# Optimization experiments

Hardware: AMD Instinct MI355X
Metric: run time of the kernel (lower is better)

The kernel has to match this reference:

```python
import jax, jax.numpy as jnp
import numpy as np

B, N, E, A, H, F, HEADS = 2, 16384, 262144, 3, 128, 16, 4
DH = H // HEADS
CONST = (2.0 * np.pi) ** 0.5


def setup_inputs() -> dict:
    key = jax.random.key(0)
    ks = jax.random.split(key, 16)
    s = 0.05
    return {
        "x": jax.random.normal(ks[0], (B, N, H), jnp.float32),
        "edge_index": jax.random.randint(ks[1], (2, E), 0, N),
        # per-action message MLPs (self.mlp)
        "mlp_W1": jax.random.normal(ks[2], (A, H, H), jnp.float32) * s,
        "mlp_b1": jnp.zeros((A, H), jnp.float32),
        "mlp_W2": jax.random.normal(ks[3], (A, H, H), jnp.float32) * s,
        "mlp_b2": jnp.zeros((A, H), jnp.float32),
        # transformer (MMTs) projections, 4 heads over the action axis
        "Wq": jax.random.normal(ks[4], (H, H), jnp.float32) * s,
        "bq": jnp.zeros((H,), jnp.float32),
        "Wk": jax.random.normal(ks[5], (H, H), jnp.float32) * s,
        "bk": jnp.zeros((H,), jnp.float32),
        "Wv": jax.random.normal(ks[6], (H, H), jnp.float32) * s,
        "bv": jnp.zeros((H,), jnp.float32),
        "Wo": jax.random.normal(ks[7], (H, H), jnp.float32) * s,
        "bo": jnp.zeros((H,), jnp.float32),
        # decide_mu MLPs (decide_In_sigma is never used in the original forward)
        "mu_W1": jax.random.normal(ks[8], (A, H, H), jnp.float32) * s,
        "mu_b1": jnp.zeros((A, H), jnp.float32),
        "mu_W2": jax.random.normal(ks[9], (A, H, F), jnp.float32) * s,
        "mu_b2": jnp.zeros((A, F), jnp.float32),
    }


def _forward(x, edge_index, mlp_W1, mlp_b1, mlp_W2, mlp_b2,
             Wq, bq, Wk, bk, Wv, bv, Wo, bo, mu_W1, mu_b1, mu_W2, mu_b2):
    # per-action MLP stack: (B,N,H) -> (B,N,A,H)
    h = jax.nn.relu(jnp.einsum('bnh,ahk->bnak', x, mlp_W1) + mlp_b1)
    h = jnp.einsum('bnak,akh->bnah', h, mlp_W2) + mlp_b2
    # gather along source nodes, scatter-add into destination bins
    dst, src = edge_index[0], edge_index[1]
    g = h[:, src]                                   # (B,E,A,H) ~ 800 MB
    agg = jax.ops.segment_sum(jnp.moveaxis(g, 1, 0), dst, num_segments=N)
    agg = jnp.moveaxis(agg, 0, 1)                   # (B,N,A,H)
    # multi-head self-attention over the action axis (len A) per node
    q = (jnp.einsum('bnah,hk->bnak', agg, Wq) + bq).reshape(B, N, A, HEADS, DH)
    k = (jnp.einsum('bnah,hk->bnak', agg, Wk) + bk).reshape(B, N, A, HEADS, DH)
    v = (jnp.einsum('bnah,hk->bnak', agg, Wv) + bv).reshape(B, N, A, HEADS, DH)
    scores = jnp.einsum('bnqed,bnked->bneqk', q, k) / (DH ** 0.5)
    attn = jax.nn.softmax(scores, axis=-1)
    o = jnp.einsum('bneqk,bnked->bnqed', attn, v).reshape(B, N, A, H)
    h_I = agg + jnp.einsum('bnah,hk->bnak', o, Wo) + bo  # residual
    # per-action decode to action means: (B,N,A,F)
    m = jax.nn.relu(jnp.einsum('bnah,ahk->bnak', h_I, mu_W1) + mu_b1)
    mu = jnp.einsum('bnak,akf->bnaf', m, mu_W2) + mu_b2
    # Gaussian reparameterized sampling, VAR is a non-trainable all-ones buffer
    VAR = jnp.ones((N, A, F), jnp.float32)
    noise = jax.random.normal(jax.random.key(42), mu.shape, mu.dtype)
    sample = mu + noise * VAR
    logp = -jnp.log(CONST * VAR) - (sample - mu) ** 2 / (2.0 * VAR ** 2)
    a0 = jax.nn.softmax(jnp.tanh(sample[:, :, 0, :]), axis=-1)
    a1 = jax.nn.sigmoid(sample[:, :, 1, :])
    a2 = jnp.tanh(sample[:, :, 2, :])
    sample_out = jnp.stack([a0, a1, a2], axis=2)    # (B,N,A,F)
    return sample_out, logp.sum((-1, -2))           # ((B,N,A,F),(B,N))


def reference(x, edge_index, mlp_W1, mlp_b1, mlp_W2, mlp_b2,
              Wq, bq, Wk, bk, Wv, bv, Wo, bo, mu_W1, mu_b1, mu_W2, mu_b2):
    return _forward(x, edge_index, mlp_W1, mlp_b1, mlp_W2, mlp_b2,
                    Wq, bq, Wk, bk, Wv, bv, Wo, bo, mu_W1, mu_b1, mu_W2, mu_b2)
```

## Files before the change

### kernel.cpp

```cpp
#include <hip/hip_runtime.h>
#include <hip/hip_bf16.h>

#define NN    16384
#define EE    262144
#define BNODES 32768
#define AH    384
#define TOT_NOISE 1572864u

typedef __attribute__((ext_vector_type(8))) short short8;
typedef __attribute__((ext_vector_type(4))) float v4f;
typedef __attribute__((ext_vector_type(2))) float f32x2;

__device__ __forceinline__ unsigned short f2bf(float f) {
  unsigned u = __float_as_uint(f);
  unsigned r = u + 0x7fffu + ((u >> 16) & 1u);
  return (unsigned short)(r >> 16);
}
__device__ __forceinline__ float bf2f(unsigned short h) {
  return __uint_as_float(((unsigned)h) << 16);
}
__device__ __forceinline__ float bflo(unsigned u) { return __uint_as_float(u << 16); }
__device__ __forceinline__ float bfhi(unsigned u) { return __uint_as_float(u & 0xffff0000u); }
__device__ __forceinline__ unsigned pk_bf16(float a, float b) {
  __hip_bfloat162 h = __float22bfloat162_rn(make_float2(a, b));
  return *(unsigned*)&h;
}

__device__ __forceinline__ void threefry2x32_042(unsigned& x0, unsigned& x1) {
  const unsigned ks0 = 0u;
  const unsigned ks1 = 42u;
  const unsigned ks2 = 0x1BD11BDAu ^ 0u ^ 42u;
  x0 += ks0; x1 += ks1;
#define TFR(r) { x0 += x1; x1 = (x1 << (r)) | (x1 >> (32 - (r))); x1 ^= x0; }
  TFR(13) TFR(15) TFR(26) TFR(6)   x0 += ks1; x1 += ks2 + 1u;
  TFR(17) TFR(29) TFR(16) TFR(24)  x0 += ks2; x1 += ks0 + 2u;
  TFR(13) TFR(15) TFR(26) TFR(6)   x0 += ks0; x1 += ks1 + 3u;
  TFR(17) TFR(29) TFR(16) TFR(24)  x0 += ks1; x1 += ks2 + 4u;
  TFR(13) TFR(15) TFR(26) TFR(6)   x0 += ks2; x1 += ks0 + 5u;
#undef TFR
}

__device__ __forceinline__ float erfinv_f32(float x) {
  float w = -log1pf(-x * x);
  float p;
  if (w < 5.0f) {
    w -= 2.5f;
    p = 2.81022636e-08f;
    p = fmaf(p, w, 3.43273939e-07f);
    p = fmaf(p, w, -3.5233877e-06f);
    p = fmaf(p, w, -4.39150654e-06f);
    p = fmaf(p, w, 0.00021858087f);
    p = fmaf(p, w, -0.00125372503f);
    p = fmaf(p, w, -0.00417768164f);
    p = fmaf(p, w, 0.246640727f);
    p = fmaf(p, w, 1.50140941f);
  } else {
    w = sqrtf(w) - 3.0f;
    p = -0.000200214257f;
    p = fmaf(p, w, 0.000100950558f);
    p = fmaf(p, w, 0.00134934322f);
    p = fmaf(p, w, -0.00367342844f);
    p = fmaf(p, w, 0.00573950773f);
    p = fmaf(p, w, -0.0076224613f);
    p = fmaf(p, w, 0.00943887047f);
    p = fmaf(p, w, 1.00167406f);
    p = fmaf(p, w, 2.83297682f);
  }
  return p * x;
}

__device__ __forceinline__ unsigned jax_random_bits32(unsigned i) {
  unsigned x0 = 0u, x1 = i;
  threefry2x32_042(x0, x1);
  return x0 ^ x1;
}

__device__ __forceinline__ float jax_normal_from_bits(unsigned bits) {
  float f = __uint_as_float((bits >> 9) | 0x3f800000u) - 1.0f;
  const float lo = -0.99999994f;
  float u = f * 2.0f + lo;
  u = fmaxf(u, lo);
  return 1.4142135623730951f * erfinv_f32(u);
}

__global__ void edge_count(const int* __restrict__ dst, int* __restrict__ deg) {
  int e = blockIdx.x * 256 + threadIdx.x;
  if (e < EE) atomicAdd(&deg[dst[e]], 1);
}

__global__ __launch_bounds__(1024) void scan_k(const int* __restrict__ deg,
                                               int* __restrict__ offs,
                                               int* __restrict__ cur) {
  __shared__ int wsum[16];
  const int t = threadIdx.x;
  const int base = t * 16;
  int loc[16];
  int s = 0;
#pragma unroll
  for (int i = 0; i < 16; i++) { loc[i] = deg[base + i]; s += loc[i]; }
  const int mysum = s;
  const int lane = t & 63, wid = t >> 6;
#pragma unroll
  for (int off = 1; off < 64; off <<= 1) {
    int v = __shfl_up(s, off, 64);
    if (lane >= off) s += v;
  }
  if (lane == 63) wsum[wid] = s;
  __syncthreads();
  if (t == 0) {
    int r = 0;
#pragma unroll
    for (int i = 0; i < 16; i++) { int v = wsum[i]; wsum[i] = r; r += v; }
  }
  __syncthreads();
  int run = wsum[wid] + s - mysum;
#pragma unroll
  for (int i = 0; i < 16; i++) {
    offs[base + i] = run;
    cur[base + i] = run;
    run += loc[i];
  }
  if (t == 1023) offs[NN] = run;
}

__global__ void edge_fill(const int* __restrict__ dst, const int* __restrict__ srcv,
                          int* __restrict__ cur, int* __restrict__ csr) {
  int e = blockIdx.x * 256 + threadIdx.x;
  if (e < EE) {
    int d = dst[e];
    int p = atomicAdd(&cur[d], 1);
    csr[p] = srcv[e];
  }
}

__global__ __launch_bounds__(256) void prep_wfrag(
    const float* __restrict__ W1, const float* __restrict__ W2,
    const float* __restrict__ mW1,
    const float* __restrict__ Wq, const float* __restrict__ Wk,
    const float* __restrict__ Wv, const float* __restrict__ Wo,
    const float* __restrict__ mW2,
    unsigned short* __restrict__ F) {
  int m = blockIdx.y;
  int f = blockIdx.x * 256 + threadIdx.x;
  if (m == 13) {
    if (f < 6144) {
      int a = f >> 11;
      int r2 = f & 2047;
      int kt = r2 >> 9;
      int r = r2 & 511;
      int lane = r >> 3, j = r & 7;
      int k = kt * 32 + (lane >> 4) * 8 + j;
      int n = lane & 15;
      F[13 * 16384 + f] = f2bf(mW2[(a * 128 + k) * 16 + n]);
    }
    return;
  }
  const float* W;
  if (m < 3) W = W1 + (long)m * 16384;
  else if (m < 6) W = W2 + (long)(m - 3) * 16384;
  else if (m < 9) W = mW1 + (long)(m - 6) * 16384;
  else W = (m == 9) ? Wq : (m == 10) ? Wk : (m == 11) ? Wv : Wo;
  int tile = f >> 9;
  int kt = tile >> 3, nt = tile & 7;
  int r = f & 511;
  int lane = r >> 3, j = r & 7;
  int k = kt * 32 + (lane >> 4) * 8 + j;
  int n = nt * 16 + (lane & 15);
  F[(long)m * 16384 + f] = f2bf(W[k * 128 + n]);
}

#define GXSTR 136
__global__ __launch_bounds__(256, 4) void mlp_fused(
    const float* __restrict__ X,
    const unsigned short* __restrict__ WF1, const float* __restrict__ b1,
    const unsigned short* __restrict__ WF2, const float* __restrict__ b2,
    unsigned short* __restrict__ H) {
  __shared__ __align__(16) unsigned short As[128 * GXSTR];
  const int a = blockIdx.y;
  const long m0 = (long)blockIdx.x * 128;
  const int tid = threadIdx.x;
  const unsigned short* Wp1 = WF1 + (long)a * 16384;
  const unsigned short* Wp2 = WF2 + (long)a * 16384;

#pragma unroll
  for (int p = 0; p < 8; p++) {
    int c = tid + p * 256;
    int row = c >> 4, c8 = (c & 15) * 8;
    float4 v1 = *(const float4*)(X + (m0 + row) * 128 + c8);
    float4 v2 = *(const float4*)(X + (m0 + row) * 128 + c8 + 4);
    uint4 o = make_uint4(pk_bf16(v1.x, v1.y), pk_bf16(v1.z, v1.w),
                         pk_bf16(v2.x, v2.y), pk_bf16(v2.z, v2.w));
    *(uint4*)(&As[row * GXSTR + c8]) = o;
  }
  __syncthreads();

  const int w = tid >> 6, l = tid & 63, lr = l & 15, lg = l >> 4;

  v4f acc[8][2];
#pragma unroll
  for (int mt = 0; mt < 8; mt++) {
    acc[mt][0] = (v4f){0.f, 0.f, 0.f, 0.f};
    acc[mt][1] = (v4f){0.f, 0.f, 0.f, 0.f};
  }
#pragma unroll
  for (int kt = 0; kt < 4; kt++) {
    short8 bfr[2];
#pragma unroll
    for (int ntl = 0; ntl < 2; ntl++)
      bfr[ntl] = *(const short8*)(Wp1 + (long)(kt * 8 + 2 * w + ntl) * 512 + l * 8);
#pragma unroll
    for (int mt = 0; mt < 8; mt++) {
      short8 af = *(const short8*)(&As[(mt * 16 + lr) * GXSTR + kt * 32 + lg * 8]);
      acc[mt][0] = __builtin_amdgcn_mfma_f32_16x16x32_bf16(af, bfr[0], acc[mt][0], 0, 0, 0);
      acc[mt][1] = __builtin_amdgcn_mfma_f32_16x16x32_bf16(af, bfr[1], acc[mt][1], 0, 0, 0);
    }
  }
  __syncthreads();

  {
    float bv[2] = {b1[a * 128 + 32 * w + lr], b1[a * 128 + 32 * w + 16 + lr]};
#pragma unroll
    for (int mt = 0; mt < 8; mt++)
#pragma unroll
      for (int ntl = 0; ntl < 2; ntl++)
#pragma unroll
        for (int i = 0; i < 4; i++) {
          int row = mt * 16 + lg * 4 + i;
          int col = 32 * w + ntl * 16 + lr;
          As[row * GXSTR + col] = f2bf(fmaxf(acc[mt][ntl][i] + bv[ntl], 0.0f));
        }
  }
  __syncthreads();

#pragma unroll
  for (int mt = 0; mt < 8; mt++) {
    acc[mt][0] = (v4f){0.f, 0.f, 0.f, 0.f};
    acc[mt][1] = (v4f){0.f, 0.f, 0.f, 0.f};
  }
#pragma unroll
  for (int kt = 0; kt < 4; kt++) {
    short8 bfr[2];
#pragma unroll
    for (int ntl = 0; ntl < 2; ntl++)
      bfr[ntl] = *(const short8*)(Wp2 + (long)(kt * 8 + 2 * w + ntl) * 512 + l * 8);
#pragma unroll
    for (int mt = 0; mt < 8; mt++) {
      short8 af = *(const short8*)(&As[(mt * 16 + lr) * GXSTR + kt * 32 + lg * 8]);
      acc[mt][0] = __builtin_amdgcn_mfma_f32_16x16x32_bf16(af, bfr[0], acc[mt][0], 0, 0, 0);
      acc[mt][1] = __builtin_amdgcn_mfma_f32_16x16x32_bf16(af, bfr[1], acc[mt][1], 0, 0, 0);
    }
  }
  {
    float bv[2] = {b2[a * 128 + 32 * w + lr], b2[a * 128 + 32 * w + 16 + lr]};
#pragma unroll
    for (int mt = 0; mt < 8; mt++)
#pragma unroll
      for (int ntl = 0; ntl < 2; ntl++)
#pragma unroll
        for (int i = 0; i < 4; i++) {
          long row = m0 + mt * 16 + lg * 4 + i;
          int col = 32 * w + ntl * 16 + lr;
          H[row * 384 + a * 128 + col] = f2bf(acc[mt][ntl][i] + bv[ntl]);
        }
  }
}

#define XSTR 136
#define QSTR 34
__global__ __launch_bounds__(256, 3) void attn_mega(
    const unsigned short* __restrict__ H, const int* __restrict__ offs,
    const int* __restrict__ csr,
    const unsigned short* __restrict__ WF,
    const float* __restrict__ bq, const float* __restrict__ bk,
    const float* __restrict__ bv, const float* __restrict__ bo,
    const unsigned short* __restrict__ WM1, const float* __restrict__ mb1,
    const unsigned short* __restrict__ WM2, const float* __restrict__ mb2,
    float* __restrict__ out0, float* __restrict__ out1) {
  __shared__ __align__(16) unsigned short xS[48 * XSTR];
  __shared__ __align__(16) unsigned short kS[4 * 48 * QSTR];
  __shared__ __align__(16) unsigned short vS[4 * 48 * QSTR];
  __shared__ float lpS[48];

  const int tid = threadIdx.x;
  const long node0 = (long)blockIdx.x * 16;

  {
    const int bt = (int)(node0 >> 14);
    const int nbase = (int)(node0 & (NN - 1));
    const int nd = tid >> 4;
    const int sub = tid & 15;
    const int n = nbase + nd;
    const int e0 = offs[n], e1 = offs[n + 1];
    const int cnt = e1 - e0;
    const unsigned short* hb = H + (long)bt * NN * 384 + sub * 24;
    f32x2 acc12[12];
#pragma unroll
    for (int i = 0; i < 12; i++) acc12[i] = (f32x2){0.f, 0.f};

    int i0, i1, i2, i3;
    { int a_ = e0 + sub;      a_ = (a_ < EE) ? a_ : (EE - 1); i0 = csr[a_]; }
    { int a_ = e0 + 16 + sub; a_ = (a_ < EE) ? a_ : (EE - 1); i1 = csr[a_]; }
    { int a_ = e0 + 32 + sub; a_ = (a_ < EE) ? a_ : (EE - 1); i2 = csr[a_]; }
    { int a_ = e0 + 48 + sub; a_ = (a_ < EE) ? a_ : (EE - 1); i3 = csr[a_]; }

#define ACC8(bp, u)                                                     \
    { acc12[bp+0] += (f32x2){bflo(u.x), bfhi(u.x)};                     \
      acc12[bp+1] += (f32x2){bflo(u.y), bfhi(u.y)};                     \
      acc12[bp+2] += (f32x2){bflo(u.z), bfhi(u.z)};                     \
      acc12[bp+3] += (f32x2){bflo(u.w), bfhi(u.w)}; }
#define GACC(BUF, KK)                                                   \
    if ((KK) < cnt) { ACC8(0, BUF##0) ACC8(4, BUF##1) ACC8(8, BUF##2) }
#define ROWLD(BUF, SPTR)                                                \
    { const unsigned short* p_ = hb + (long)(SPTR) * 384;               \
      BUF##0 = *(const uint4*)(p_);                                     \
      BUF##1 = *(const uint4*)(p_ + 8);                                 \
      BUF##2 = *(const uint4*)(p_ + 16); }
#define SWZ(reg, k) __builtin_amdgcn_ds_swizzle(reg, ((k) << 5) | 16)
#define IDXG(reg, k, e) (((e) < cnt) ? SWZ(reg, k) : 0)
#define BLOCK16(b, ic, in)                                              \
    GACC(A, (b)+0)  ROWLD(A, IDXG(ic, 4,  (b)+4))                       \
    GACC(B, (b)+1)  ROWLD(B, IDXG(ic, 5,  (b)+5))                       \
    GACC(C, (b)+2)  ROWLD(C, IDXG(ic, 6,  (b)+6))                       \
    GACC(D, (b)+3)  ROWLD(D, IDXG(ic, 7,  (b)+7))                       \
    GACC(A, (b)+4)  ROWLD(A, IDXG(ic, 8,  (b)+8))                       \
    GACC(B, (b)+5)  ROWLD(B, IDXG(ic, 9,  (b)+9))                       \
    GACC(C, (b)+6)  ROWLD(C, IDXG(ic, 10, (b)+10))                      \
    GACC(D, (b)+7)  ROWLD(D, IDXG(ic, 11, (b)+11))                      \
    GACC(A, (b)+8)  ROWLD(A, IDXG(ic, 12, (b)+12))                      \
    GACC(B, (b)+9)  ROWLD(B, IDXG(ic, 13, (b)+13))                      \
    GACC(C, (b)+10) ROWLD(C, IDXG(ic, 14, (b)+14))                      \
    GACC(D, (b)+11) ROWLD(D, IDXG(ic, 15, (b)+15))                      \
    GACC(A, (b)+12) ROWLD(A, IDXG(in, 0,  (b)+16))                      \
    GACC(B, (b)+13) ROWLD(B, IDXG(in, 1,  (b)+17))                      \
    GACC(C, (b)+14) ROWLD(C, IDXG(in, 2,  (b)+18))                      \
    GACC(D, (b)+15) ROWLD(D, IDXG(in, 3,  (b)+19))

    uint4 A0, A1, A2, B0, B1, B2, C0, C1, C2, D0, D1, D2;
    {
      int t0 = IDXG(i0, 0, 0), t1 = IDXG(i0, 1, 1);
      int t2 = IDXG(i0, 2, 2), t3 = IDXG(i0, 3, 3);
      ROWLD(A, t0) ROWLD(B, t1) ROWLD(C, t2) ROWLD(D, t3)
    }
    BLOCK16(0, i0, i1)
    if (cnt > 16) {
      BLOCK16(16, i1, i2)
      if (cnt > 32) {
        BLOCK16(32, i2, i3)
        if (cnt > 48) {
          BLOCK16(48, i3, i3)
        }
      }
    }
    if (cnt > 64) {
      for (int e = 64; e < cnt; e++) {
        int s0 = csr[e0 + e];
        const unsigned short* p0 = hb + (long)s0 * 384;
        uint4 F0 = *(const uint4*)(p0);
        uint4 F1 = *(const uint4*)(p0 + 8);
        uint4 F2 = *(const uint4*)(p0 + 16);
        ACC8(0, F0) ACC8(4, F1) ACC8(8, F2)
      }
    }
#undef BLOCK16
#undef IDXG
#undef SWZ
#undef ROWLD
#undef GACC
#undef ACC8
#pragma unroll
    for (int jj = 0; jj < 12; jj++) {
      int g = sub * 24 + 2 * jj;
      int a_ = g >> 7;
      int c = g & 127;
      *(unsigned*)&xS[(3 * nd + a_) * XSTR + c] =
          pk_bf16(acc12[jj].x, acc12[jj].y);
    }
  }
  __syncthreads();

  const int w = tid >> 6;
  const int l = tid & 63;
  const int lr = l & 15;
  const int lg = l >> 4;
  const unsigned short* WQ = WF;
  const unsigned short* WK = WF + 16384;
  const unsigned short* WV = WF + 32768;
  const unsigned short* WO = WF + 49152;

  v4f accq[3][2], acck[3][2], accv[3][2];
#pragma unroll
  for (int mt = 0; mt < 3; mt++)
#pragma unroll
    for (int n = 0; n < 2; n++) {
      accq[mt][n] = (v4f){0.f, 0.f, 0.f, 0.f};
      acck[mt][n] = (v4f){0.f, 0.f, 0.f, 0.f};
      accv[mt][n] = (v4f){0.f, 0.f, 0.f, 0.f};
    }
#pragma unroll
  for (int kt = 0; kt < 4; kt++) {
    short8 af[3];
#pragma unroll
    for (int mt = 0; mt < 3; mt++)
      af[mt] = *(const short8*)&xS[(mt * 16 + lr) * XSTR + kt * 32 + lg * 8];
#pragma unroll
    for (int ntl = 0; ntl < 2; ntl++) {
      long tf = (long)(kt * 8 + 2 * w + ntl) * 512 + l * 8;
      short8 b0 = *(const short8*)&WQ[tf];
      short8 b1 = *(const short8*)&WK[tf];
      short8 b2 = *(const short8*)&WV[tf];
#pragma unroll
      for (int mt = 0; mt < 3; mt++) {
        accq[mt][ntl] = __builtin_amdgcn_mfma_f32_16x16x32_bf16(af[mt], b0, accq[mt][ntl], 0, 0, 0);
        acck[mt][ntl] = __builtin_amdgcn_mfma_f32_16x16x32_bf16(af[mt], b1, acck[mt][ntl], 0, 0, 0);
        accv[mt][ntl] = __builtin_amdgcn_mfma_f32_16x16x32_bf16(af[mt], b2, accv[mt][ntl], 0, 0, 0);
      }
    }
  }
  __syncthreads();

  float resv[3][2][4];
#pragma unroll
  for (int mt = 0; mt < 3; mt++)
#pragma unroll
    for (int ntl = 0; ntl < 2; ntl++)
#pragma unroll
      for (int i = 0; i < 4; i++)
        resv[mt][ntl][i] =
            bf2f(xS[(mt * 16 + lg * 4 + i) * XSTR + 32 * w + ntl * 16 + lr]);

  {
    const float scale = 0.17677669529663687f;
    unsigned short* kw = &kS[w * 48 * QSTR];
    unsigned short* vw = &vS[w * 48 * QSTR];
    float bqv[2] = {bq[32 * w + lr], bq[32 * w + 16 + lr]};
    float bkv[2] = {bk[32 * w + lr], bk[32 * w + 16 + lr]};
    float bvv[2] = {bv[32 * w + lr], bv[32 * w + 16 + lr]};
#pragma unroll
    for (int mt = 0; mt < 3; mt++)
#pragma unroll
      for (int ntl = 0; ntl < 2; ntl++)
#pragma unroll
        for (int i = 0; i < 4; i++) {
          int row = mt * 16 + lg * 4 + i;
          int col = ntl * 16 + lr;
          xS[row * XSTR + 32 * w + col] = f2bf((accq[mt][ntl][i] + bqv[ntl]) * scale);
          kw[row * QSTR + col] = f2bf(acck[mt][ntl][i] + bkv[ntl]);
          vw[row * QSTR + col] = f2bf(accv[mt][ntl][i] + bvv[ntl]);
        }
  }
  __syncthreads();

  if (l < 48) {
    int aq = l % 3;
    int ndr = l - aq;
    const unsigned* qr = (const unsigned*)&xS[l * XSTR + 32 * w];
    const unsigned* kr0 = (const unsigned*)&kS[(w * 48 + ndr) * QSTR];
    const unsigned* kr1 = (const unsigned*)&kS[(w * 48 + ndr + 1) * QSTR];
    const unsigned* kr2 = (const unsigned*)&kS[(w * 48 + ndr + 2) * QSTR];
// ... 73 lines not shown
  for (int mt = 0; mt < 3; mt++)
#pragma unroll
    for (int n = 0; n < 2; n++) accm[mt][n] = (v4f){0.f, 0.f, 0.f, 0.f};
#pragma unroll
  for (int kt = 0; kt < 4; kt++) {
#pragma unroll
    for (int mt = 0; mt < 3; mt++) {
      short8 af = *(const short8*)&xS[(mt * 16 + lr) * XSTR + kt * 32 + lg * 8];
#pragma unroll
      for (int ntl = 0; ntl < 2; ntl++) {
        short8 b = *(const short8*)(WM1 + (long)mt * 16384 +
                                    (long)(kt * 8 + 2 * w + ntl) * 512 + l * 8);
        accm[mt][ntl] = __builtin_amdgcn_mfma_f32_16x16x32_bf16(af, b, accm[mt][ntl], 0, 0, 0);
      }
    }
  }
  __syncthreads();

#pragma unroll
  for (int mt = 0; mt < 3; mt++)
#pragma unroll
    for (int ntl = 0; ntl < 2; ntl++) {
      int col = 32 * w + ntl * 16 + lr;
      float bias = mb1[mt * 128 + col];
#pragma unroll
      for (int i = 0; i < 4; i++) {
        int rowp = mt * 16 + lg * 4 + i;
        xS[rowp * XSTR + col] = f2bf(fmaxf(accm[mt][ntl][i] + bias, 0.0f));
      }
    }
  __syncthreads();

  if (w < 3) {
    v4f accu = (v4f){0.f, 0.f, 0.f, 0.f};
#pragma unroll
    for (int kt = 0; kt < 4; kt++) {
      short8 af = *(const short8*)&xS[(w * 16 + lr) * XSTR + kt * 32 + lg * 8];
      short8 b = *(const short8*)(WM2 + w * 2048 + kt * 512 + l * 8);
      accu = __builtin_amdgcn_mfma_f32_16x16x32_bf16(af, b, accu, 0, 0, 0);
    }
    float bias = mb2[w * 16 + lr];
#pragma unroll
    for (int i = 0; i < 4; i++) {
      int nd = lg * 4 + i;
      float mu = accu[i] + bias;
      unsigned gidx = (unsigned)((node0 + nd) * 48 + w * 16 + lr);
      unsigned bits = jax_random_bits32(gidx);
      float noise = jax_normal_from_bits(bits);
      float sample = mu + noise;
      float lp = -0.9189385332046727f - 0.5f * noise * noise;
      lp += __shfl_xor(lp, 1, 64);
      lp += __shfl_xor(lp, 2, 64);
      lp += __shfl_xor(lp, 4, 64);
      lp += __shfl_xor(lp, 8, 64);
      if (lr == 0) lpS[w * 16 + nd] = lp;
      float res;
      if (w == 0) {
        float th = tanhf(sample);
        float mx = th;
        mx = fmaxf(mx, __shfl_xor(mx, 1, 64));
        mx = fmaxf(mx, __shfl_xor(mx, 2, 64));
        mx = fmaxf(mx, __shfl_xor(mx, 4, 64));
        mx = fmaxf(mx, __shfl_xor(mx, 8, 64));
        float ex = expf(th - mx);
        float ss = ex;
        ss += __shfl_xor(ss, 1, 64);
        ss += __shfl_xor(ss, 2, 64);
        ss += __shfl_xor(ss, 4, 64);
        ss += __shfl_xor(ss, 8, 64);
        res = ex / ss;
      } else if (w == 1) {
        res = 1.0f / (1.0f + expf(-sample));
      } else {
        res = tanhf(sample);
      }
      out0[gidx] = res;
    }
  }
  __syncthreads();
  if (tid < 16)
    out1[node0 + tid] = lpS[tid] + lpS[16 + tid] + lpS[32 + tid];
}

extern "C" void kernel_launch(void* const* d_in, const int* in_sizes, int n_in,
                              void* d_out, int out_size, void* d_ws, size_t ws_size,
                              hipStream_t stream) {
  const float* x = (const float*)d_in[0];
  const int* ei = (const int*)d_in[1];
  const float* W1 = (const float*)d_in[2];
  const float* b1 = (const float*)d_in[3];
  const float* W2 = (const float*)d_in[4];
  const float* b2 = (const float*)d_in[5];
  const float* Wq = (const float*)d_in[6];
  const float* bq = (const float*)d_in[7];
  const float* Wk = (const float*)d_in[8];
  const float* bk = (const float*)d_in[9];
  const float* Wv = (const float*)d_in[10];
  const float* bv = (const float*)d_in[11];
  const float* Wo = (const float*)d_in[12];
  const float* bo = (const float*)d_in[13];
  const float* mW1 = (const float*)d_in[14];
  const float* mb1 = (const float*)d_in[15];
  const float* mW2 = (const float*)d_in[16];
  const float* mb2 = (const float*)d_in[17];
  (void)in_sizes; (void)n_in; (void)out_size; (void)ws_size;

  unsigned short* HB = (unsigned short*)d_ws;
  int* deg = (int*)(HB + 12582912);
  int* offs = deg + NN;
  int* cur = offs + (NN + 1);
  int* csr = cur + NN;
  unsigned short* wfrag = (unsigned short*)(((uintptr_t)(csr + EE) + 15) & ~(uintptr_t)15);
  unsigned short* w2frag = wfrag + 13 * 16384;

  const int* dst = ei;
  const int* srcv = ei + EE;

  float* out0 = (float*)d_out;
  float* out1 = out0 + TOT_NOISE;

  hipMemsetAsync(deg, 0, NN * sizeof(int), stream);
  edge_count<<<EE / 256, 256, 0, stream>>>(dst, deg);
  scan_k<<<1, 1024, 0, stream>>>(deg, offs, cur);
  edge_fill<<<EE / 256, 256, 0, stream>>>(dst, srcv, cur, csr);
  prep_wfrag<<<dim3(64, 14), 256, 0, stream>>>(W1, W2, mW1, Wq, Wk, Wv, Wo, mW2, wfrag);

  mlp_fused<<<dim3(BNODES / 128, 3), 256, 0, stream>>>(x, wfrag, b1, wfrag + 3 * 16384, b2, HB);
  attn_mega<<<BNODES / 16, 256, 0, stream>>>(HB, offs, csr,
                                             wfrag + 9 * 16384, bq, bk, bv, bo,
                                             wfrag + 6 * 16384, mb1, w2frag, mb2,
                                             out0, out1);
}
```

Measured before the change: 225.8 us.

## Split gather from attention kernel to raise gather occupancy

Splits the fused gather+attention kernel into a standalone gather kernel, launch-bounded for 8 blocks per CU with a shallower 2-deep load pipeline, and a post kernel that reads the aggregated bf16 rows from a new workspace buffer. The aim is to let the latency-bound random gather run at higher occupancy instead of being capped by the attention kernel's register and LDS use. In exchange, the aggregate (about 25 MB in bf16) makes an extra round trip through global memory and there is one more launch. The fused kernel is kept as a fallback when the workspace is too small.

```diff
diff --git a/kernel.cpp b/kernel.cpp
--- a/kernel.cpp
+++ b/kernel.cpp
@@ -265,43 +265,26 @@
   }
 }
 
-#define XSTR 136
-#define QSTR 34
-__global__ __launch_bounds__(256, 3) void attn_mega(
+__global__ __launch_bounds__(256, 8) void gather_k(
     const unsigned short* __restrict__ H, const int* __restrict__ offs,
-    const int* __restrict__ csr,
-    const unsigned short* __restrict__ WF,
-    const float* __restrict__ bq, const float* __restrict__ bk,
-    const float* __restrict__ bv, const float* __restrict__ bo,
-    const unsigned short* __restrict__ WM1, const float* __restrict__ mb1,
-    const unsigned short* __restrict__ WM2, const float* __restrict__ mb2,
-    float* __restrict__ out0, float* __restrict__ out1) {
-  __shared__ __align__(16) unsigned short xS[48 * XSTR];
-  __shared__ __align__(16) unsigned short kS[4 * 48 * QSTR];
-  __shared__ __align__(16) unsigned short vS[4 * 48 * QSTR];
-  __shared__ float lpS[48];
-
+    const int* __restrict__ csr, unsigned short* __restrict__ AGG) {
   const int tid = threadIdx.x;
   const long node0 = (long)blockIdx.x * 16;
-
-  {
-    const int bt = (int)(node0 >> 14);
-    const int nbase = (int)(node0 & (NN - 1));
-    const int nd = tid >> 4;
-    const int sub = tid & 15;
-    const int n = nbase + nd;
-    const int e0 = offs[n], e1 = offs[n + 1];
-    const int cnt = e1 - e0;
-    const unsigned short* hb = H + (long)bt * NN * 384 + sub * 24;
-    f32x2 acc12[12];
-#pragma unroll
-    for (int i = 0; i < 12; i++) acc12[i] = (f32x2){0.f, 0.f};
-
-    int i0, i1, i2, i3;
-    { int a_ = e0 + sub;      a_ = (a_ < EE) ? a_ : (EE - 1); i0 = csr[a_]; }
-    { int a_ = e0 + 16 + sub; a_ = (a_ < EE) ? a_ : (EE - 1); i1 = csr[a_]; }
-    { int a_ = e0 + 32 + sub; a_ = (a_ < EE) ? a_ : (EE - 1); i2 = csr[a_]; }
-    { int a_ = e0 + 48 + sub; a_ = (a_ < EE) ? a_ : (EE - 1); i3 = csr[a_]; }
+  const int bt = (int)(node0 >> 14);
+  const int nbase = (int)(node0 & (NN - 1));
+  const int nd = tid >> 4;
+  const int sub = tid & 15;
+  const int n = nbase + nd;
+  const int e0 = offs[n], e1 = offs[n + 1];
+  const int cnt = e1 - e0;
+  const unsigned short* hb = H + (long)bt * NN * 384 + sub * 24;
+  f32x2 acc12[12];
+#pragma unroll
+  for (int i = 0; i < 12; i++) acc12[i] = (f32x2){0.f, 0.f};
+
+  int i0, i1;
+  { int a_ = e0 + sub;      a_ = (a_ < EE) ? a_ : (EE - 1); i0 = csr[a_]; }
+  { int a_ = e0 + 16 + sub; a_ = (a_ < EE) ? a_ : (EE - 1); i1 = csr[a_]; }
 
 #define ACC8(bp, u)                                                     \
     { acc12[bp+0] += (f32x2){bflo(u.x), bfhi(u.x)};                     \
@@ -317,42 +300,34 @@
       BUF##2 = *(const uint4*)(p_ + 16); }
 #define SWZ(reg, k) __builtin_amdgcn_ds_swizzle(reg, ((k) << 5) | 16)
 #define IDXG(reg, k, e) (((e) < cnt) ? SWZ(reg, k) : 0)
-#define BLOCK16(b, ic, in)                                              \
-    GACC(A, (b)+0)  ROWLD(A, IDXG(ic, 4,  (b)+4))                       \
-    GACC(B, (b)+1)  ROWLD(B, IDXG(ic, 5,  (b)+5))                       \
-    GACC(C, (b)+2)  ROWLD(C, IDXG(ic, 6,  (b)+6))                       \
-    GACC(D, (b)+3)  ROWLD(D, IDXG(ic, 7,  (b)+7))                       \
-    GACC(A, (b)+4)  ROWLD(A, IDXG(ic, 8,  (b)+8))                       \
-    GACC(B, (b)+5)  ROWLD(B, IDXG(ic, 9,  (b)+9))                       \
-    GACC(C, (b)+6)  ROWLD(C, IDXG(ic, 10, (b)+10))                      \
-    GACC(D, (b)+7)  ROWLD(D, IDXG(ic, 11, (b)+11))                      \
-    GACC(A, (b)+8)  ROWLD(A, IDXG(ic, 12, (b)+12))                      \
-    GACC(B, (b)+9)  ROWLD(B, IDXG(ic, 13, (b)+13))                      \
-    GACC(C, (b)+10) ROWLD(C, IDXG(ic, 14, (b)+14))                      \
-    GACC(D, (b)+11) ROWLD(D, IDXG(ic, 15, (b)+15))                      \
-    GACC(A, (b)+12) ROWLD(A, IDXG(in, 0,  (b)+16))                      \
-    GACC(B, (b)+13) ROWLD(B, IDXG(in, 1,  (b)+17))                      \
-    GACC(C, (b)+14) ROWLD(C, IDXG(in, 2,  (b)+18))                      \
-    GACC(D, (b)+15) ROWLD(D, IDXG(in, 3,  (b)+19))
-
-    uint4 A0, A1, A2, B0, B1, B2, C0, C1, C2, D0, D1, D2;
-    {
-      int t0 = IDXG(i0, 0, 0), t1 = IDXG(i0, 1, 1);
-      int t2 = IDXG(i0, 2, 2), t3 = IDXG(i0, 3, 3);
-      ROWLD(A, t0) ROWLD(B, t1) ROWLD(C, t2) ROWLD(D, t3)
-    }
-    BLOCK16(0, i0, i1)
-    if (cnt > 16) {
-      BLOCK16(16, i1, i2)
-      if (cnt > 32) {
-        BLOCK16(32, i2, i3)
-        if (cnt > 48) {
-          BLOCK16(48, i3, i3)
-        }
-      }
-    }
-    if (cnt > 64) {
-      for (int e = 64; e < cnt; e++) {
+#define BLOCK16_D2(b, ic, in)                                           \
+    GACC(A, (b)+0)  ROWLD(A, IDXG(ic, 2,  (b)+2))                       \
+    GACC(B, (b)+1)  ROWLD(B, IDXG(ic, 3,  (b)+3))                       \
+    GACC(A, (b)+2)  ROWLD(A, IDXG(ic, 4,  (b)+4))                       \
+    GACC(B, (b)+3)  ROWLD(B, IDXG(ic, 5,  (b)+5))                       \
+    GACC(A, (b)+4)  ROWLD(A, IDXG(ic, 6,  (b)+6))                       \
+    GACC(B, (b)+5)  ROWLD(B, IDXG(ic, 7,  (b)+7))                       \
+    GACC(A, (b)+6)  ROWLD(A, IDXG(ic, 8,  (b)+8))                       \
+    GACC(B, (b)+7)  ROWLD(B, IDXG(ic, 9,  (b)+9))                       \
+    GACC(A, (b)+8)  ROWLD(A, IDXG(ic, 10, (b)+10))                      \
+    GACC(B, (b)+9)  ROWLD(B, IDXG(ic, 11, (b)+11))                      \
+    GACC(A, (b)+10) ROWLD(A, IDXG(ic, 12, (b)+12))                      \
+    GACC(B, (b)+11) ROWLD(B, IDXG(ic, 13, (b)+13))                      \
+    GACC(A, (b)+12) ROWLD(A, IDXG(ic, 14, (b)+14))                      \
+    GACC(B, (b)+13) ROWLD(B, IDXG(ic, 15, (b)+15))                      \
+    GACC(A, (b)+14) ROWLD(A, IDXG(in, 0,  (b)+16))                      \
+    GACC(B, (b)+15) ROWLD(B, IDXG(in, 1,  (b)+17))
+
+  uint4 A0, A1, A2, B0, B1, B2;
+  {
+    int t0 = IDXG(i0, 0, 0), t1 = IDXG(i0, 1, 1);
+    ROWLD(A, t0) ROWLD(B, t1)
+  }
+  BLOCK16_D2(0, i0, i1)
+  if (cnt > 16) {
+    BLOCK16_D2(16, i1, i1)
+    if (cnt > 32) {
+      for (int e = 32; e < cnt; e++) {
         int s0 = csr[e0 + e];
         const unsigned short* p0 = hb + (long)s0 * 384;
         uint4 F0 = *(const uint4*)(p0);
@@ -361,19 +336,66 @@
         ACC8(0, F0) ACC8(4, F1) ACC8(8, F2)
       }
     }
-#undef BLOCK16
+  }
+#undef BLOCK16_D2
 #undef IDXG
 #undef SWZ
 #undef ROWLD
 #undef GACC
 #undef ACC8
+
+  uint4 o0 = make_uint4(pk_bf16(acc12[0].x, acc12[0].y),
+                        pk_bf16(acc12[1].x, acc12[1].y),
+                        pk_bf16(acc12[2].x, acc12[2].y),
+                        pk_bf16(acc12[3].x, acc12[3].y));
+  uint4 o1 = make_uint4(pk_bf16(acc12[4].x, acc12[4].y),
+                        pk_bf16(acc12[5].x, acc12[5].y),
+                        pk_bf16(acc12[6].x, acc12[6].y),
+                        pk_bf16(acc12[7].x, acc12[7].y));
+  uint4 o2 = make_uint4(pk_bf16(acc12[8].x, acc12[8].y),
+                        pk_bf16(acc12[9].x, acc12[9].y),
+                        pk_bf16(acc12[10].x, acc12[10].y),
+                        pk_bf16(acc12[11].x, acc12[11].y));
+  unsigned short* op = AGG + (node0 + (long)nd) * 384 + sub * 24;
+  *(uint4*)(op) = o0;
+  *(uint4*)(op + 8) = o1;
+  *(uint4*)(op + 16) = o2;
+}
+
+#define XSTR 136
+#define QSTR 34
+__global__ __launch_bounds__(256, 3) void attn_post(
+    const unsigned short* __restrict__ AGG,
+    const unsigned short* __restrict__ WF,
+    const float* __restrict__ bq, const float* __restrict__ bk,
+    const float* __restrict__ bv, const float* __restrict__ bo,
+    const unsigned short* __restrict__ WM1, const float* __restrict__ mb1,
+    const unsigned short* __restrict__ WM2, const float* __restrict__ mb2,
+    float* __restrict__ out0, float* __restrict__ out1) {
+  __shared__ __align__(16) unsigned short xS[48 * XSTR];
+  __shared__ __align__(16) unsigned short kS[4 * 48 * QSTR];
+  __shared__ __align__(16) unsigned short vS[4 * 48 * QSTR];
+  __shared__ float lpS[48];
+
+  const int tid = threadIdx.x;
+  const long node0 = (long)blockIdx.x * 16;
+
+  {
+    const int nd = tid >> 4;
+    const int sub = tid & 15;
+    const unsigned short* ag = AGG + (node0 + (long)nd) * 384 + sub * 24;
+    uint4 r0 = *(const uint4*)(ag);
+    uint4 r1 = *(const uint4*)(ag + 8);
+    uint4 r2 = *(const uint4*)(ag + 16);
+    unsigned pr[12] = {r0.x, r0.y, r0.z, r0.w,
+                       r1.x, r1.y, r1.z, r1.w,
+                       r2.x, r2.y, r2.z, r2.w};
 #pragma unroll
     for (int jj = 0; jj < 12; jj++) {
       int g = sub * 24 + 2 * jj;
       int a_ = g >> 7;
       int c = g & 127;
-      *(unsigned*)&xS[(3 * nd + a_) * XSTR + c] =
-          pk_bf16(acc12[jj].x, acc12[jj].y);
+      *(unsigned*)&xS[(3 * nd + a_) * XSTR + c] = pr[jj];
     }
   }
   __syncthreads();
@@ -613,6 +635,352 @@
     out1[node0 + tid] = lpS[tid] + lpS[16 + tid] + lpS[32 + tid];
 }
 
+__global__ __launch_bounds__(256, 3) void attn_mega(
+    const unsigned short* __restrict__ H, const int* __restrict__ offs,
+    const int* __restrict__ csr,
+    const unsigned short* __restrict__ WF,
+    const float* __restrict__ bq, const float* __restrict__ bk,
+    const float* __restrict__ bv, const float* __restrict__ bo,
+    const unsigned short* __restrict__ WM1, const float* __restrict__ mb1,
+    const unsigned short* __restrict__ WM2, const float* __restrict__ mb2,
+    float* __restrict__ out0, float* __restrict__ out1) {
+  __shared__ __align__(16) unsigned short xS[48 * XSTR];
+  __shared__ __align__(16) unsigned short kS[4 * 48 * QSTR];
+  __shared__ __align__(16) unsigned short vS[4 * 48 * QSTR];
+  __shared__ float lpS[48];
+
+  const int tid = threadIdx.x;
+  const long node0 = (long)blockIdx.x * 16;
+
+  {
+    const int bt = (int)(node0 >> 14);
+    const int nbase = (int)(node0 & (NN - 1));
+    const int nd = tid >> 4;
+    const int sub = tid & 15;
+    const int n = nbase + nd;
+    const int e0 = offs[n], e1 = offs[n + 1];
+    const int cnt = e1 - e0;
+    const unsigned short* hb = H + (long)bt * NN * 384 + sub * 24;
+    f32x2 acc12[12];
+#pragma unroll
+    for (int i = 0; i < 12; i++) acc12[i] = (f32x2){0.f, 0.f};
+
+    int i0, i1, i2, i3;
+    { int a_ = e0 + sub;      a_ = (a_ < EE) ? a_ : (EE - 1); i0 = csr[a_]; }
+    { int a_ = e0 + 16 + sub; a_ = (a_ < EE) ? a_ : (EE - 1); i1 = csr[a_]; }
+    { int a_ = e0 + 32 + sub; a_ = (a_ < EE) ? a_ : (EE - 1); i2 = csr[a_]; }
+    { int a_ = e0 + 48 + sub; a_ = (a_ < EE) ? a_ : (EE - 1); i3 = csr[a_]; }
+
+#define ACC8(bp, u)                                                     \
+    { acc12[bp+0] += (f32x2){bflo(u.x), bfhi(u.x)};                     \
+      acc12[bp+1] += (f32x2){bflo(u.y), bfhi(u.y)};                     \
+      acc12[bp+2] += (f32x2){bflo(u.z), bfhi(u.z)};                     \
+      acc12[bp+3] += (f32x2){bflo(u.w), bfhi(u.w)}; }
+#define GACC(BUF, KK)                                                   \
+    if ((KK) < cnt) { ACC8(0, BUF##0) ACC8(4, BUF##1) ACC8(8, BUF##2) }
+#define ROWLD(BUF, SPTR)                                                \
+    { const unsigned short* p_ = hb + (long)(SPTR) * 384;               \
+      BUF##0 = *(const uint4*)(p_);                                     \
+      BUF##1 = *(const uint4*)(p_ + 8);                                 \
+      BUF##2 = *(const uint4*)(p_ + 16); }
+#define SWZ(reg, k) __builtin_amdgcn_ds_swizzle(reg, ((k) << 5) | 16)
+#define IDXG(reg, k, e) (((e) < cnt) ? SWZ(reg, k) : 0)
+#define BLOCK16(b, ic, in)                                              \
+    GACC(A, (b)+0)  ROWLD(A, IDXG(ic, 4,  (b)+4))                       \
+    GACC(B, (b)+1)  ROWLD(B, IDXG(ic, 5,  (b)+5))                       \
+    GACC(C, (b)+2)  ROWLD(C, IDXG(ic, 6,  (b)+6))                       \
+    GACC(D, (b)+3)  ROWLD(D, IDXG(ic, 7,  (b)+7))                       \
+    GACC(A, (b)+4)  ROWLD(A, IDXG(ic, 8,  (b)+8))                       \
+    GACC(B, (b)+5)  ROWLD(B, IDXG(ic, 9,  (b)+9))                       \
+    GACC(C, (b)+6)  ROWLD(C, IDXG(ic, 10, (b)+10))                      \
+    GACC(D, (b)+7)  ROWLD(D, IDXG(ic, 11, (b)+11))                      \
+    GACC(A, (b)+8)  ROWLD(A, IDXG(ic, 12, (b)+12))                      \
+    GACC(B, (b)+9)  ROWLD(B, IDXG(ic, 13, (b)+13))                      \
+    GACC(C, (b)+10) ROWLD(C, IDXG(ic, 14, (b)+14))                      \
+    GACC(D, (b)+11) ROWLD(D, IDXG(ic, 15, (b)+15))                      \
+    GACC(A, (b)+12) ROWLD(A, IDXG(in, 0,  (b)+16))                      \
+    GACC(B, (b)+13) ROWLD(B, IDXG(in, 1,  (b)+17))                      \
+    GACC(C, (b)+14) ROWLD(C, IDXG(in, 2,  (b)+18))                      \
+    GACC(D, (b)+15) ROWLD(D, IDXG(in, 3,  (b)+19))
+
+    uint4 A0, A1, A2, B0, B1, B2, C0, C1, C2, D0, D1, D2;
+    {
+      int t0 = IDXG(i0, 0, 0), t1 = IDXG(i0, 1, 1);
+      int t2 = IDXG(i0, 2, 2), t3 = IDXG(i0, 3, 3);
+      ROWLD(A, t0) ROWLD(B, t1) ROWLD(C, t2) ROWLD(D, t3)
+    }
+    BLOCK16(0, i0, i1)
+    if (cnt > 16) {
+      BLOCK16(16, i1, i2)
+      if (cnt > 32) {
+        BLOCK16(32, i2, i3)
+        if (cnt > 48) {
+          BLOCK16(48, i3, i3)
+        }
+      }
+    }
+    if (cnt > 64) {
+      for (int e = 64; e < cnt; e++) {
+        int s0 = csr[e0 + e];
+        const unsigned short* p0 = hb + (long)s0 * 384;
+        uint4 F0 = *(const uint4*)(p0);
+        uint4 F1 = *(const uint4*)(p0 + 8);
+        uint4 F2 = *(const uint4*)(p0 + 16);
+        ACC8(0, F0) ACC8(4, F1) ACC8(8, F2)
+      }
+    }
+#undef BLOCK16
+#undef IDXG
+#undef SWZ
+#undef ROWLD
+#undef GACC
+#undef ACC8
+#pragma unroll
+    for (int jj = 0; jj < 12; jj++) {
+      int g = sub * 24 + 2 * jj;
+      int a_ = g >> 7;
+      int c = g & 127;
+      *(unsigned*)&xS[(3 * nd + a_) * XSTR + c] =
+          pk_bf16(acc12[jj].x, acc12[jj].y);
+    }
+  }
+  __syncthreads();
+
+  const int w = tid >> 6;
+  const int l = tid & 63;
+  const int lr = l & 15;
+  const int lg = l >> 4;
+  const unsigned short* WQ = WF;
+  const unsigned short* WK = WF + 16384;
+  const unsigned short* WV = WF + 32768;
+  const unsigned short* WO = WF + 49152;
+
+  v4f accq[3][2], acck[3][2], accv[3][2];
+#pragma unroll
+  for (int mt = 0; mt < 3; mt++)
+#pragma unroll
+    for (int n = 0; n < 2; n++) {
+      accq[mt][n] = (v4f){0.f, 0.f, 0.f, 0.f};
+      acck[mt][n] = (v4f){0.f, 0.f, 0.f, 0.f};
+      accv[mt][n] = (v4f){0.f, 0.f, 0.f, 0.f};
+    }
+#pragma unroll
+  for (int kt = 0; kt < 4; kt++) {
+    short8 af[3];
+#pragma unroll
+    for (int mt = 0; mt < 3; mt++)
+      af[mt] = *(const short8*)&xS[(mt * 16 + lr) * XSTR + kt * 32 + lg * 8];
+#pragma unroll
+    for (int ntl = 0; ntl < 2; ntl++) {
+      long tf = (long)(kt * 8 + 2 * w + ntl) * 512 + l * 8;
+      short8 b0 = *(const short8*)&WQ[tf];
+      short8 b1 = *(const short8*)&WK[tf];
+      short8 b2 = *(const short8*)&WV[tf];
+#pragma unroll
+      for (int mt = 0; mt < 3; mt++) {
+        accq[mt][ntl] = __builtin_amdgcn_mfma_f32_16x16x32_bf16(af[mt], b0, accq[mt][ntl], 0, 0, 0);
+        acck[mt][ntl] = __builtin_amdgcn_mfma_f32_16x16x32_bf16(af[mt], b1, acck[mt][ntl], 0, 0, 0);
+        accv[mt][ntl] = __builtin_amdgcn_mfma_f32_16x16x32_bf16(af[mt], b2, accv[mt][ntl], 0, 0, 0);
+      }
+    }
+  }
+  __syncthreads();
+
+  float resv[3][2][4];
+#pragma unroll
+  for (int mt = 0; mt < 3; mt++)
+#pragma unroll
+    for (int ntl = 0; ntl < 2; ntl++)
+#pragma unroll
+      for (int i = 0; i < 4; i++)
+        resv[mt][ntl][i] =
+            bf2f(xS[(mt * 16 + lg * 4 + i) * XSTR + 32 * w + ntl * 16 + lr]);
+
+  {
+    const float scale = 0.17677669529663687f;
+    unsigned short* kw = &kS[w * 48 * QSTR];
+    unsigned short* vw = &vS[w * 48 * QSTR];
+    float bqv[2] = {bq[32 * w + lr], bq[32 * w + 16 + lr]};
+    float bkv[2] = {bk[32 * w + lr], bk[32 * w + 16 + lr]};
+    float bvv[2] = {bv[32 * w + lr], bv[32 * w + 16 + lr]};
+#pragma unroll
+    for (int mt = 0; mt < 3; mt++)
+#pragma unroll
+      for (int ntl = 0; ntl < 2; ntl++)
+#pragma unroll
+        for (int i = 0; i < 4; i++) {
+          int row = mt * 16 + lg * 4 + i;
+          int col = ntl * 16 + lr;
+          xS[row * XSTR + 32 * w + col] = f2bf((accq[mt][ntl][i] + bqv[ntl]) * scale);
+          kw[row * QSTR + col] = f2bf(acck[mt][ntl][i] + bkv[ntl]);
+          vw[row * QSTR + col] = f2bf(accv[mt][ntl][i] + bvv[ntl]);
+        }
+  }
+  __syncthreads();
+
+  if (l < 48) {
+    int aq = l % 3;
+    int ndr = l - aq;
+    const unsigned* qr = (const unsigned*)&xS[l * XSTR + 32 * w];
+    const unsigned* kr0 = (const unsigned*)&kS[(w * 48 + ndr) * QSTR];
+    const unsigned* kr1 = (const unsigned*)&kS[(w * 48 + ndr + 1) * QSTR];
+    const unsigned* kr2 = (const unsigned*)&kS[(w * 48 + ndr + 2) * QSTR];
+    float s0 = 0.f, s1 = 0.f, s2 = 0.f;
+#pragma unroll
+    for (int j = 0; j < 16; j++) {
+      unsigned uq = qr[j], u0 = kr0[j], u1 = kr1[j], u2 = kr2[j];
+      float qa = bflo(uq), qb = bfhi(uq);
+      s0 = fmaf(qa, bflo(u0), fmaf(qb, bfhi(u0), s0));
+      s1 = fmaf(qa, bflo(u1), fmaf(qb, bfhi(u1), s1));
+      s2 = fmaf(qa, bflo(u2), fmaf(qb, bfhi(u2), s2));
+    }
+    float mx = fmaxf(s0, fmaxf(s1, s2));
+    float e0 = expf(s0 - mx), e1 = expf(s1 - mx), e2 = expf(s2 - mx);
+    float inv = 1.0f / (e0 + e1 + e2);
+    e0 *= inv; e1 *= inv; e2 *= inv;
+    const unsigned* vr0 = (const unsigned*)&vS[(w * 48 + ndr) * QSTR];
+    const unsigned* vr1 = (const unsigned*)&vS[(w * 48 + ndr + 1) * QSTR];
+    const unsigned* vr2 = (const unsigned*)&vS[(w * 48 + ndr + 2) * QSTR];
+    unsigned ov[16];
+#pragma unroll
+    for (int j = 0; j < 16; j++) {
+      unsigned u0 = vr0[j], u1 = vr1[j], u2 = vr2[j];
+      float oa = fmaf(e0, bflo(u0), fmaf(e1, bflo(u1), e2 * bflo(u2)));
+      float ob = fmaf(e0, bfhi(u0), fmaf(e1, bfhi(u1), e2 * bfhi(u2)));
+      ov[j] = pk_bf16(oa, ob);
+    }
+    uint4* orow = (uint4*)&xS[l * XSTR + 32 * w];
+    orow[0] = make_uint4(ov[0], ov[1], ov[2], ov[3]);
+    orow[1] = make_uint4(ov[4], ov[5], ov[6], ov[7]);
+    orow[2] = make_uint4(ov[8], ov[9], ov[10], ov[11]);
+    orow[3] = make_uint4(ov[12], ov[13], ov[14], ov[15]);
+  }
+  __syncthreads();
+
+  v4f acco[3][2];
+#pragma unroll
+  for (int mt = 0; mt < 3; mt++)
+#pragma unroll
+    for (int n = 0; n < 2; n++) acco[mt][n] = (v4f){0.f, 0.f, 0.f, 0.f};
+#pragma unroll
+  for (int kt = 0; kt < 4; kt++) {
+    short8 af[3];
+#pragma unroll
+    for (int mt = 0; mt < 3; mt++)
+      af[mt] = *(const short8*)&xS[(mt * 16 + lr) * XSTR + kt * 32 + lg * 8];
+#pragma unroll
+    for (int ntl = 0; ntl < 2; ntl++) {
+      long tf = (long)(kt * 8 + 2 * w + ntl) * 512 + l * 8;
+      short8 b = *(const short8*)&WO[tf];
+#pragma unroll
+      for (int mt = 0; mt < 3; mt++)
+        acco[mt][ntl] = __builtin_amdgcn_mfma_f32_16x16x32_bf16(af[mt], b, acco[mt][ntl], 0, 0, 0);
+    }
+  }
+  __syncthreads();
+
+  {
+    float bov[2] = {bo[32 * w + lr], bo[32 * w + 16 + lr]};
+#pragma unroll
+    for (int mt = 0; mt < 3; mt++)
+#pragma unroll
+      for (int ntl = 0; ntl < 2; ntl++)
+#pragma unroll
+        for (int i = 0; i < 4; i++) {
+          int row = mt * 16 + lg * 4 + i;
+          int nd = row / 3, a_ = row - nd * 3;
+          int gcol = 32 * w + ntl * 16 + lr;
+          xS[(a_ * 16 + nd) * XSTR + gcol] =
+              f2bf(acco[mt][ntl][i] + bov[ntl] + resv[mt][ntl][i]);
+        }
+  }
+  __syncthreads();
+
+  v4f accm[3][2];
+#pragma unroll
+  for (int mt = 0; mt < 3; mt++)
+#pragma unroll
+    for (int n = 0; n < 2; n++) accm[mt][n] = (v4f){0.f, 0.f, 0.f, 0.f};
+#pragma unroll
+  for (int kt = 0; kt < 4; kt++) {
+#pragma unroll
+    for (int mt = 0; mt < 3; mt++) {
+      short8 af = *(const short8*)&xS[(mt * 16 + lr) * XSTR + kt * 32 + lg * 8];
+#pragma unroll
+      for (int ntl = 0; ntl < 2; ntl++) {
+        short8 b = *(const short8*)(WM1 + (long)mt * 16384 +
+                                    (long)(kt * 8 + 2 * w + ntl) * 512 + l * 8);
+        accm[mt][ntl] = __builtin_amdgcn_mfma_f32_16x16x32_bf16(af, b, accm[mt][ntl], 0, 0, 0);
+      }
+    }
+  }
+  __syncthreads();
+
+#pragma unroll
+  for (int mt = 0; mt < 3; mt++)
+#pragma unroll
+    for (int ntl = 0; ntl < 2; ntl++) {
+      int col = 32 * w + ntl * 16 + lr;
+      float bias = mb1[mt * 128 + col];
+#pragma unroll
+      for (int i = 0; i < 4; i++) {
+        int rowp = mt * 16 + lg * 4 + i;
+        xS[rowp * XSTR + col] = f2bf(fmaxf(accm[mt][ntl][i] + bias, 0.0f));
+      }
+    }
+  __syncthreads();
+
+  if (w < 3) {
+    v4f accu = (v4f){0.f, 0.f, 0.f, 0.f};
+#pragma unroll
+    for (int kt = 0; kt < 4; kt++) {
+      short8 af = *(const short8*)&xS[(w * 16 + lr) * XSTR + kt * 32 + lg * 8];
+      short8 b = *(const short8*)(WM2 + w * 2048 + kt * 512 + l * 8);
+      accu = __builtin_amdgcn_mfma_f32_16x16x32_bf16(af, b, accu, 0, 0, 0);
+    }
+    float bias = mb2[w * 16 + lr];
+#pragma unroll
+    for (int i = 0; i < 4; i++) {
+      int nd = lg * 4 + i;
+      float mu = accu[i] + bias;
+      unsigned gidx = (unsigned)((node0 + nd) * 48 + w * 16 + lr);
+      unsigned bits = jax_random_bits32(gidx);
+      float noise = jax_normal_from_bits(bits);
+      float sample = mu + noise;
+      float lp = -0.9189385332046727f - 0.5f * noise * noise;
+      lp += __shfl_xor(lp, 1, 64);
+      lp += __shfl_xor(lp, 2, 64);
+      lp += __shfl_xor(lp, 4, 64);
+      lp += __shfl_xor(lp, 8, 64);
+      if (lr == 0) lpS[w * 16 + nd] = lp;
+      float res;
+      if (w == 0) {
+        float th = tanhf(sample);
+        float mx = th;
+        mx = fmaxf(mx, __shfl_xor(mx, 1, 64));
+        mx = fmaxf(mx, __shfl_xor(mx, 2, 64));
+        mx = fmaxf(mx, __shfl_xor(mx, 4, 64));
+        mx = fmaxf(mx, __shfl_xor(mx, 8, 64));
+        float ex = expf(th - mx);
+        float ss = ex;
+        ss += __shfl_xor(ss, 1, 64);
+        ss += __shfl_xor(ss, 2, 64);
+        ss += __shfl_xor(ss, 4, 64);
+        ss += __shfl_xor(ss, 8, 64);
+        res = ex / ss;
+      } else if (w == 1) {
+        res = 1.0f / (1.0f + expf(-sample));
+      } else {
+        res = tanhf(sample);
+      }
+      out0[gidx] = res;
+    }
+  }
+  __syncthreads();
+  if (tid < 16)
+    out1[node0 + tid] = lpS[tid] + lpS[16 + tid] + lpS[32 + tid];
+}
+
 extern "C" void kernel_launch(void* const* d_in, const int* in_sizes, int n_in,
                               void* d_out, int out_size, void* d_ws, size_t ws_size,
                               hipStream_t stream) {
@@ -634,7 +1002,7 @@
   const float* mb1 = (const float*)d_in[15];
   const float* mW2 = (const float*)d_in[16];
   const float* mb2 = (const float*)d_in[17];
-  (void)in_sizes; (void)n_in; (void)out_size; (void)ws_size;
+  (void)in_sizes; (void)n_in; (void)out_size;
 
   unsigned short* HB = (unsigned short*)d_ws;
   int* deg = (int*)(HB + 12582912);
@@ -643,6 +1011,8 @@
   int* csr = cur + NN;
   unsigned short* wfrag = (unsigned short*)(((uintptr_t)(csr + EE) + 15) & ~(uintptr_t)15);
   unsigned short* w2frag = wfrag + 13 * 16384;
+  unsigned short* aggB = (unsigned short*)(((uintptr_t)(w2frag + 6144) + 15) & ~(uintptr_t)15);
+  size_t needed = (size_t)((char*)(aggB + 12582912) - (char*)d_ws);
 
   const int* dst = ei;
   const int* srcv = ei + EE;
@@ -657,8 +1027,17 @@
   prep_wfrag<<<dim3(64, 14), 256, 0, stream>>>(W1, W2, mW1, Wq, Wk, Wv, Wo, mW2, wfrag);
 
   mlp_fused<<<dim3(BNODES / 128, 3), 256, 0, stream>>>(x, wfrag, b1, wfrag + 3 * 16384, b2, HB);
-  attn_mega<<<BNODES / 16, 256, 0, stream>>>(HB, offs, csr,
-                                             wfrag + 9 * 16384, bq, bk, bv, bo,
-                                             wfrag + 6 * 16384, mb1, w2frag, mb2,
-                                             out0, out1);
-}
+
+  if (ws_size >= needed) {
+    gather_k<<<BNODES / 16, 256, 0, stream>>>(HB, offs, csr, aggB);
+    attn_post<<<BNODES / 16, 256, 0, stream>>>(aggB,
+                                               wfrag + 9 * 16384, bq, bk, bv, bo,
+                                               wfrag + 6 * 16384, mb1, w2frag, mb2,
+                                               out0, out1);
+  } else {
+    attn_mega<<<BNODES / 16, 256, 0, stream>>>(HB, offs, csr,
+                                               wfrag + 9 * 16384, bq, bk, bv, bo,
+                                               wfrag + 6 * 16384, mb1, w2frag, mb2,
+                                               out0, out1);
+  }
+}
```

Result: slower. 239.5 us (+6.0%).

## Merge independent preprocessing kernels into shared launches by block-index partitioning

Applied to the files above, without the earlier changes.

Folds the edge degree counting into the weight-fragment prep kernel, and the CSR fill into the MLP kernel, using block-index ranges to pick the role. Launches drop from six kernels to four. Independent work also runs side by side in one grid. The CSR-fill blocks now share a grid with the heavier MLP blocks, which have shared-memory and launch-bound constraints, so occupancy for the light atomic blocks may be limited.

```diff
diff --git a/kernel.cpp b/kernel.cpp
--- a/kernel.cpp
+++ b/kernel.cpp
@@ -83,11 +83,6 @@
   return 1.4142135623730951f * erfinv_f32(u);
 }
 
-__global__ void edge_count(const int* __restrict__ dst, int* __restrict__ deg) {
-  int e = blockIdx.x * 256 + threadIdx.x;
-  if (e < EE) atomicAdd(&deg[dst[e]], 1);
-}
-
 __global__ __launch_bounds__(1024) void scan_k(const int* __restrict__ deg,
                                                int* __restrict__ offs,
                                                int* __restrict__ cur) {
@@ -123,25 +118,23 @@
   if (t == 1023) offs[NN] = run;
 }
 
-__global__ void edge_fill(const int* __restrict__ dst, const int* __restrict__ srcv,
-                          int* __restrict__ cur, int* __restrict__ csr) {
-  int e = blockIdx.x * 256 + threadIdx.x;
-  if (e < EE) {
-    int d = dst[e];
-    int p = atomicAdd(&cur[d], 1);
-    csr[p] = srcv[e];
-  }
-}
-
-__global__ __launch_bounds__(256) void prep_wfrag(
+__global__ __launch_bounds__(256) void cp_fused(
+    const int* __restrict__ dst, int* __restrict__ deg,
     const float* __restrict__ W1, const float* __restrict__ W2,
     const float* __restrict__ mW1,
     const float* __restrict__ Wq, const float* __restrict__ Wk,
     const float* __restrict__ Wv, const float* __restrict__ Wo,
     const float* __restrict__ mW2,
     unsigned short* __restrict__ F) {
-  int m = blockIdx.y;
-  int f = blockIdx.x * 256 + threadIdx.x;
+  const int b = blockIdx.x;
+  if (b < 1024) {
+    int e = b * 256 + threadIdx.x;
+    if (e < EE) atomicAdd(&deg[dst[e]], 1);
+    return;
+  }
+  const int pb = b - 1024;
+  const int m = pb >> 6;
+  const int f = (pb & 63) * 256 + threadIdx.x;
   if (m == 13) {
     if (f < 6144) {
       int a = f >> 11;
@@ -170,15 +163,28 @@
 }
 
 #define GXSTR 136
-__global__ __launch_bounds__(256, 4) void mlp_fused(
+__global__ __launch_bounds__(256, 4) void fm_fused(
+    const int* __restrict__ dst, const int* __restrict__ srcv,
+    int* __restrict__ cur, int* __restrict__ csr,
     const float* __restrict__ X,
     const unsigned short* __restrict__ WF1, const float* __restrict__ b1,
     const unsigned short* __restrict__ WF2, const float* __restrict__ b2,
     unsigned short* __restrict__ H) {
   __shared__ __align__(16) unsigned short As[128 * GXSTR];
-  const int a = blockIdx.y;
-  const long m0 = (long)blockIdx.x * 128;
+  const int blk = blockIdx.x;
   const int tid = threadIdx.x;
+  if (blk < 1024) {
+    int e = blk * 256 + tid;
+    if (e < EE) {
+      int d = dst[e];
+      int p = atomicAdd(&cur[d], 1);
+      csr[p] = srcv[e];
+    }
+    return;
+  }
+  const int pb = blk - 1024;
+  const int a = pb >> 8;
+  const long m0 = (long)(pb & 255) * 128;
   const unsigned short* Wp1 = WF1 + (long)a * 16384;
   const unsigned short* Wp2 = WF2 + (long)a * 16384;
 
@@ -651,12 +657,11 @@
   float* out1 = out0 + TOT_NOISE;
 
   hipMemsetAsync(deg, 0, NN * sizeof(int), stream);
-  edge_count<<<EE / 256, 256, 0, stream>>>(dst, deg);
+  cp_fused<<<1920, 256, 0, stream>>>(dst, deg, W1, W2, mW1, Wq, Wk, Wv, Wo,
+                                     mW2, wfrag);
   scan_k<<<1, 1024, 0, stream>>>(deg, offs, cur);
-  edge_fill<<<EE / 256, 256, 0, stream>>>(dst, srcv, cur, csr);
-  prep_wfrag<<<dim3(64, 14), 256, 0, stream>>>(W1, W2, mW1, Wq, Wk, Wv, Wo, mW2, wfrag);
-
-  mlp_fused<<<dim3(BNODES / 128, 3), 256, 0, stream>>>(x, wfrag, b1, wfrag + 3 * 16384, b2, HB);
+  fm_fused<<<1792, 256, 0, stream>>>(dst, srcv, cur, csr,
+                                     x, wfrag, b1, wfrag + 3 * 16384, b2, HB);
   attn_mega<<<BNODES / 16, 256, 0, stream>>>(HB, offs, csr,
                                              wfrag + 9 * 16384, bq, bk, bv, bo,
                                              wfrag + 6 * 16384, mb1, w2frag, mb2,
```

Measured after the change: 225.4 us (median of 2 runs). About the same (-0.2%).
